# Performance work log

Measured on AMD Instinct MI355X. Metric: run time of the kernel, lower is better.

The kernel has to match this reference:

```python
import jax, jax.numpy as jnp
import numpy as np

B, D, H, W = 16, 512, 64, 64
K = 64  # clusters
EPS = 1e-12  # torch F.normalize eps


def _l2norm(v, axis):
    n = jnp.linalg.norm(v, axis=axis, keepdims=True)
    return v / jnp.maximum(n, EPS)


def setup_inputs() -> dict:
    key = jax.random.key(0)
    k1, k2, k3, k4 = jax.random.split(key, 4)
    x = jax.random.normal(k1, (B, D, H, W), dtype=jnp.float32)
    # conv weight/bias are independent trainable params after init; sample them
    centers = jax.random.uniform(k2, (K, D), dtype=jnp.float32)
    conv_w = 2.0 * 100.0 * centers + 0.01 * jax.random.normal(k3, (K, D), dtype=jnp.float32)
    conv_b = -100.0 * jnp.linalg.norm(centers, axis=1) + 0.01 * jax.random.normal(k4, (K,), dtype=jnp.float32)
    return {"x": x, "conv_w": conv_w, "conv_b": conv_b, "centers": centers}


def reference(x, conv_w, conv_b, centers):
    b = x.shape[0]
    x_flat = x.reshape(b, D, -1)                       # (B, D, N)
    # 1x1 conv == per-location linear over channels
    logits = jnp.einsum('bdn,kd->bkn', x_flat, conv_w) + conv_b[None, :, None]
    w = jax.nn.softmax(logits, axis=1)                 # softmax over clusters
    # vlad[b,k,d] = sum_n w[b,k,n]*(x[b,d,n] - c[k,d])
    #            = (w @ x^T)[b,k,d] - (sum_n w[b,k,n]) * c[k,d]
    wx = jnp.einsum('bkn,bdn->bkd', w, x_flat)         # (B, K, D)
    wsum = jnp.sum(w, axis=-1)                          # (B, K)
    vlad = wx - wsum[:, :, None] * centers[None]        # (B, K, D)
    vlad = _l2norm(vlad, axis=2)                        # intra-normalize
    vlad = vlad.reshape(b, -1)
    vlad = _l2norm(vlad, axis=1)                        # global L2
    return vlad
```

## Files before the change

### kernel.cpp

```cpp
#include <hip/hip_runtime.h>
#include <hip/hip_bf16.h>
#include <math.h>

#define B_ 16
#define D_ 512
#define N_ 4096
#define K_ 64

typedef __attribute__((ext_vector_type(8))) short bfrag;
typedef __attribute__((ext_vector_type(4))) float f32x4;

static __device__ __forceinline__ float bf2f(unsigned short u) {
    return __uint_as_float(((unsigned)u) << 16);
}
static __device__ __forceinline__ unsigned short f2bf(float v) {
    __hip_bfloat16 h = __float2bfloat16(v);
    union { __hip_bfloat16 h; unsigned short u; } cv; cv.h = h; return cv.u;
}
static __device__ __forceinline__ void split3(float v, unsigned short& h,
                                              unsigned short& m, unsigned short& l) {
    h = f2bf(v); float r1 = v - bf2f(h);
    m = f2bf(r1); float r2 = r1 - bf2f(m);
    l = f2bf(r2);
}
static __device__ __forceinline__ void split2(float v, unsigned short& h,
                                              unsigned short& l) {
    h = f2bf(v); l = f2bf(v - bf2f(h));
}
#define MFMA(a, b, c) __builtin_amdgcn_mfma_f32_16x16x32_bf16((a), (b), (c), 0, 0, 0)

__global__ __launch_bounds__(256) void k_prep(
    const float* __restrict__ conv_w, unsigned short* __restrict__ cwL)
{
    const int i = blockIdx.x * 256 + threadIdx.x;
    const float4 v = *(const float4*)&conv_w[i * 4];
    const float vv[4] = {v.x, v.y, v.z, v.w};
    unsigned short h[4], m[4], l[4];
    #pragma unroll
    for (int j = 0; j < 4; ++j) split3(vv[j], h[j], m[j], l[j]);
    *(ushort4*)&cwL[0 * (K_ * D_) + i * 4] = make_ushort4(h[0], h[1], h[2], h[3]);
    *(ushort4*)&cwL[1 * (K_ * D_) + i * 4] = make_ushort4(m[0], m[1], m[2], m[3]);
    *(ushort4*)&cwL[2 * (K_ * D_) + i * 4] = make_ushort4(l[0], l[1], l[2], l[3]);
}

__global__ __launch_bounds__(256) void k_logits_softmax(
    const float* __restrict__ x, const unsigned short* __restrict__ cwL,
    const float* __restrict__ conv_b,
    unsigned short* __restrict__ wh, unsigned short* __restrict__ wl,
    float* __restrict__ wsumbuf)
{
    const int b   = blockIdx.x >> 5;
    const int n0  = (blockIdx.x & 31) * 128;
    const int tid  = threadIdx.x;
    const int w    = tid >> 6;
    const int lane = tid & 63;
    const int q = lane >> 4;
    const int c = lane & 15;
    const int ktb = (w & 1) * 32;
    const int ntb = (w >> 1) * 64;

    __shared__ unsigned short cws[3][64][40];
    __shared__ unsigned short xs[3][128][40];
    __shared__ float redm[2][128];
    __shared__ float reds[2][128];

    f32x4 acc[2][4];
    #pragma unroll
    for (int kt = 0; kt < 2; ++kt)
        #pragma unroll
        for (int nt = 0; nt < 4; ++nt) acc[kt][nt] = (f32x4){0.f, 0.f, 0.f, 0.f};

    const float* xb = x + (size_t)b * D_ * N_ + n0;

    const int ks = tid >> 2;
    const int d8 = (tid & 3) * 8;
    const int xn = tid & 127;
    const int xd = (tid >> 7) * 4;

    float px[16];
    uint4 pcw[3];

    auto load_step = [&](int d0) {
        #pragma unroll
        for (int lv = 0; lv < 3; ++lv)
            pcw[lv] = *(const uint4*)&cwL[lv * (K_ * D_) + ks * D_ + d0 + d8];
        #pragma unroll
        for (int i = 0; i < 4; ++i)
            #pragma unroll
            for (int r = 0; r < 4; ++r)
                px[i * 4 + r] = xb[(size_t)(d0 + 8 * i + xd + r) * N_ + xn];
    };

    load_step(0);

    for (int s = 0; s < 16; ++s) {
        #pragma unroll
        for (int lv = 0; lv < 3; ++lv)
            *(uint4*)&cws[lv][ks][d8] = pcw[lv];
        #pragma unroll
        for (int i = 0; i < 4; ++i) {
            unsigned short h[4], m[4], l[4];
            #pragma unroll
            for (int r = 0; r < 4; ++r) split3(px[i * 4 + r], h[r], m[r], l[r]);
            const int dg = 8 * i + xd;
            *(ushort4*)&xs[0][xn][dg] = make_ushort4(h[0], h[1], h[2], h[3]);
            *(ushort4*)&xs[1][xn][dg] = make_ushort4(m[0], m[1], m[2], m[3]);
            *(ushort4*)&xs[2][xn][dg] = make_ushort4(l[0], l[1], l[2], l[3]);
        }
        __syncthreads();

        if (s < 15) load_step((s + 1) * 32);

        bfrag af[2][3];
        #pragma unroll
        for (int kt = 0; kt < 2; ++kt)
            #pragma unroll
            for (int lv = 0; lv < 3; ++lv)
                af[kt][lv] = *(const bfrag*)&cws[lv][ktb + kt * 16 + c][q * 8];
        #pragma unroll
        for (int nt = 0; nt < 4; ++nt) {
            bfrag bf[3];
            #pragma unroll
            for (int lv = 0; lv < 3; ++lv)
                bf[lv] = *(const bfrag*)&xs[lv][ntb + nt * 16 + c][q * 8];
            #pragma unroll
            for (int kt = 0; kt < 2; ++kt) {
                f32x4 a = acc[kt][nt];
                a = MFMA(af[kt][0], bf[0], a);
                a = MFMA(af[kt][0], bf[1], a);
                a = MFMA(af[kt][1], bf[0], a);
                a = MFMA(af[kt][1], bf[1], a);
                a = MFMA(af[kt][0], bf[2], a);
                a = MFMA(af[kt][2], bf[0], a);
                acc[kt][nt] = a;
            }
        }
        __syncthreads();
    }

    #pragma unroll
    for (int kt = 0; kt < 2; ++kt)
        #pragma unroll
        for (int r = 0; r < 4; ++r) {
            const float bias = conv_b[ktb + kt * 16 + q * 4 + r];
            #pragma unroll
            for (int nt = 0; nt < 4; ++nt) acc[kt][nt][r] += bias;
        }

    float mloc[4];
    #pragma unroll
    for (int nt = 0; nt < 4; ++nt) {
        float m = acc[0][nt][0];
        #pragma unroll
        for (int kt = 0; kt < 2; ++kt)
            #pragma unroll
            for (int r = 0; r < 4; ++r) m = fmaxf(m, acc[kt][nt][r]);
        m = fmaxf(m, __shfl_xor(m, 16));
        m = fmaxf(m, __shfl_xor(m, 32));
        mloc[nt] = m;
    }
    if (q == 0)
        #pragma unroll
        for (int nt = 0; nt < 4; ++nt) redm[w & 1][ntb + nt * 16 + c] = mloc[nt];
    __syncthreads();
    float mall[4];
    #pragma unroll
    for (int nt = 0; nt < 4; ++nt)
        mall[nt] = fmaxf(redm[0][ntb + nt * 16 + c], redm[1][ntb + nt * 16 + c]);

    float sloc[4] = {0.f, 0.f, 0.f, 0.f};
    #pragma unroll
    for (int nt = 0; nt < 4; ++nt) {
        #pragma unroll
        for (int kt = 0; kt < 2; ++kt)
            #pragma unroll
            for (int r = 0; r < 4; ++r) {
                const float e = __expf(acc[kt][nt][r] - mall[nt]);
                acc[kt][nt][r] = e;
                sloc[nt] += e;
            }
        sloc[nt] += __shfl_xor(sloc[nt], 16);
        sloc[nt] += __shfl_xor(sloc[nt], 32);
    }
    if (q == 0)
        #pragma unroll
        for (int nt = 0; nt < 4; ++nt) reds[w & 1][ntb + nt * 16 + c] = sloc[nt];
    __syncthreads();

    float wacc[2][4] = {{0.f, 0.f, 0.f, 0.f}, {0.f, 0.f, 0.f, 0.f}};
    #pragma unroll
    for (int nt = 0; nt < 4; ++nt) {
        const float inv = 1.0f / (reds[0][ntb + nt * 16 + c] + reds[1][ntb + nt * 16 + c]);
        #pragma unroll
        for (int kt = 0; kt < 2; ++kt)
            #pragma unroll
            for (int r = 0; r < 4; ++r) {
                const float v = acc[kt][nt][r] * inv;
                unsigned short hi, lo;
                split2(v, hi, lo);
                const size_t idx = ((size_t)b * K_ + ktb + kt * 16 + q * 4 + r) * N_
                                 + n0 + ntb + nt * 16 + c;
                wh[idx] = hi;
                wl[idx] = lo;
                wacc[kt][r] += v;
            }
    }
    #pragma unroll
    for (int msk = 1; msk < 16; msk <<= 1)
        #pragma unroll
        for (int kt = 0; kt < 2; ++kt)
            #pragma unroll
            for (int r = 0; r < 4; ++r)
                wacc[kt][r] += __shfl_xor(wacc[kt][r], msk);
    if (c == 0)
        #pragma unroll
        for (int kt = 0; kt < 2; ++kt)
            #pragma unroll
            for (int r = 0; r < 4; ++r)
                atomicAdd(&wsumbuf[b * K_ + ktb + kt * 16 + q * 4 + r], wacc[kt][r]);
}

__global__ __launch_bounds__(256) void k_wx(
    const float* __restrict__ x, const unsigned short* __restrict__ wh,
    const unsigned short* __restrict__ wl, float* __restrict__ vlad)
{
    const int nc = blockIdx.x & 7;
    const int dc = (blockIdx.x >> 3) & 3;
    const int b  = blockIdx.x >> 5;
    const int tid  = threadIdx.x;
    const int w    = tid >> 6;
    const int lane = tid & 63;
    const int q = lane >> 4;
    const int c = lane & 15;
    const int ktb = (w & 1) * 32;
    const int dtb = (w >> 1) * 64;

    __shared__ unsigned short ws2[2][64][40];
    __shared__ unsigned short xs2[2][128][40];

    f32x4 acc[2][4];
    #pragma unroll
    for (int kt = 0; kt < 2; ++kt)
        #pragma unroll
        for (int dt = 0; dt < 4; ++dt) acc[kt][dt] = (f32x4){0.f, 0.f, 0.f, 0.f};

    const float* xb = x + (size_t)b * D_ * N_ + (size_t)dc * 128 * N_;
    const unsigned short* whb = wh + (size_t)b * K_ * N_;
    const unsigned short* wlb = wl + (size_t)b * K_ * N_;

    const int wk = tid >> 2;
    const int wn = (tid & 3) * 8;
    const int xd = tid >> 3;
    const int xn = (tid & 7) * 4;

    uint4 pw[2];
    float px[16];

    auto load_step = [&](int n0) {
        pw[0] = *(const uint4*)&whb[(size_t)wk * N_ + n0 + wn];
        pw[1] = *(const uint4*)&wlb[(size_t)wk * N_ + n0 + wn];
        #pragma unroll
        for (int i = 0; i < 4; ++i) {
            const float4 v = *(const float4*)&xb[(size_t)(i * 32 + xd) * N_ + n0 + xn];
            px[i * 4 + 0] = v.x; px[i * 4 + 1] = v.y;
            px[i * 4 + 2] = v.z; px[i * 4 + 3] = v.w;
        }
    };

    const int nbase = nc * 512;
    load_step(nbase);

    for (int s = 0; s < 16; ++s) {
        *(uint4*)&ws2[0][wk][wn] = pw[0];
        *(uint4*)&ws2[1][wk][wn] = pw[1];
        #pragma unroll
        for (int i = 0; i < 4; ++i) {
            unsigned short h[4], l[4];
            #pragma unroll
            for (int j = 0; j < 4; ++j) split2(px[i * 4 + j], h[j], l[j]);
            *(ushort4*)&xs2[0][i * 32 + xd][xn] = make_ushort4(h[0], h[1], h[2], h[3]);
            *(ushort4*)&xs2[1][i * 32 + xd][xn] = make_ushort4(l[0], l[1], l[2], l[3]);
        }
        __syncthreads();

        if (s < 15) load_step(nbase + (s + 1) * 32);

        bfrag afh[2], afl[2];
        #pragma unroll
        for (int kt = 0; kt < 2; ++kt) {
            afh[kt] = *(const bfrag*)&ws2[0][ktb + kt * 16 + c][q * 8];
            afl[kt] = *(const bfrag*)&ws2[1][ktb + kt * 16 + c][q * 8];
        }
        #pragma unroll
        for (int dt = 0; dt < 4; ++dt) {
            const bfrag bh = *(const bfrag*)&xs2[0][dtb + dt * 16 + c][q * 8];
            const bfrag bl = *(const bfrag*)&xs2[1][dtb + dt * 16 + c][q * 8];
            #pragma unroll
            for (int kt = 0; kt < 2; ++kt) {
                f32x4 a = acc[kt][dt];
                a = MFMA(afh[kt], bh, a);
                a = MFMA(afh[kt], bl, a);
                a = MFMA(afl[kt], bh, a);
                acc[kt][dt] = a;
            }
        }
        __syncthreads();
    }

    #pragma unroll
    for (int kt = 0; kt < 2; ++kt)
        #pragma unroll
        for (int dt = 0; dt < 4; ++dt)
            #pragma unroll
            for (int r = 0; r < 4; ++r) {
                const int k = ktb + kt * 16 + q * 4 + r;
                const int d = dc * 128 + dtb + dt * 16 + c;
                atomicAdd(&vlad[((size_t)b * K_ + k) * D_ + d], acc[kt][dt][r]);
            }
}

__global__ __launch_bounds__(256) void k_norm(
    const float* __restrict__ wsumbuf, const float* __restrict__ vlad,
    const float* __restrict__ centers, float* __restrict__ out)
{
    const int b = blockIdx.x >> 6;
    const int k = blockIdx.x & 63;
    const int tid = threadIdx.x;

    const float wsum = wsumbuf[b * K_ + k];

    const float* vr = vlad + ((size_t)b * K_ + k) * D_;
    const float* cr = centers + k * D_;
    const float v0 = vr[tid]       - wsum * cr[tid];
    const float v1 = vr[tid + 256] - wsum * cr[tid + 256];

    float ss = v0 * v0 + v1 * v1;
    __shared__ float red2[4];
    #pragma unroll
    for (int off = 32; off > 0; off >>= 1) ss += __shfl_down(ss, off, 64);
    if ((tid & 63) == 0) red2[tid >> 6] = ss;
    __syncthreads();
    const float nrm = sqrtf(red2[0] + red2[1] + red2[2] + red2[3]);
    const float scale = 1.0f / (8.0f * fmaxf(nrm, 1e-12f));

    float* outr = out + ((size_t)b * K_ + k) * D_;
    outr[tid]       = v0 * scale;
    outr[tid + 256] = v1 * scale;
}

extern "C" void kernel_launch(void* const* d_in, const int* in_sizes, int n_in,
                              void* d_out, int out_size, void* d_ws, size_t ws_size,
                              hipStream_t stream) {
    const float* x       = (const float*)d_in[0];
    const float* conv_w  = (const float*)d_in[1];
    const float* conv_b  = (const float*)d_in[2];
    const float* centers = (const float*)d_in[3];
    float* out = (float*)d_out;

    char* wsb = (char*)d_ws;
    float* vlad            = (float*)wsb;
    float* wsumbuf         = (float*)(wsb + (2u << 20));
    unsigned short* wh     = (unsigned short*)(wsb + (3u << 20));
    unsigned short* wl     = (unsigned short*)(wsb + (11u << 20));
    unsigned short* cwL    = (unsigned short*)(wsb + (19u << 20));

    hipMemsetAsync(vlad, 0, (2u << 20) + 4096, stream);

    k_prep<<<32, 256, 0, stream>>>(conv_w, cwL);
    k_logits_softmax<<<B_ * 32, 256, 0, stream>>>(x, cwL, conv_b, wh, wl, wsumbuf);
    k_wx<<<B_ * 4 * 8, 256, 0, stream>>>(x, wh, wl, vlad);
    k_norm<<<B_ * K_, 256, 0, stream>>>(wsumbuf, vlad, centers, out);
}
```

Measured before the change: 261.2 us.

## Halve tile sizes to double grid and drop register prefetch pipelining

Both GEMM kernels now use smaller per-block tiles: the logits/softmax kernel covers 64 positions per block instead of 128, and the wx kernel covers 256 positions per block instead of 512. This doubles the number of blocks to 1024 in each kernel, to fill the MI355X's CUs better. The register-level software prefetch of the next step's global loads is also removed, which cuts register pressure and should raise occupancy. The trade-off is that global-load latency is no longer overlapped with MFMA work inside a block, and the wx kernel issues twice as many atomic accumulations into vlad.

```diff
diff --git a/kernel.cpp b/kernel.cpp
--- a/kernel.cpp
+++ b/kernel.cpp
@@ -49,67 +49,53 @@
     unsigned short* __restrict__ wh, unsigned short* __restrict__ wl,
     float* __restrict__ wsumbuf)
 {
-    const int b   = blockIdx.x >> 5;
-    const int n0  = (blockIdx.x & 31) * 128;
+    const int b   = blockIdx.x >> 6;
+    const int n0  = (blockIdx.x & 63) * 64;
     const int tid  = threadIdx.x;
     const int w    = tid >> 6;
     const int lane = tid & 63;
     const int q = lane >> 4;
     const int c = lane & 15;
     const int ktb = (w & 1) * 32;
-    const int ntb = (w >> 1) * 64;
+    const int ntb = (w >> 1) * 32;
 
     __shared__ unsigned short cws[3][64][40];
-    __shared__ unsigned short xs[3][128][40];
-    __shared__ float redm[2][128];
-    __shared__ float reds[2][128];
-
-    f32x4 acc[2][4];
+    __shared__ unsigned short xs[3][64][40];
+    __shared__ float redm[2][64];
+    __shared__ float reds[2][64];
+
+    f32x4 acc[2][2];
     #pragma unroll
     for (int kt = 0; kt < 2; ++kt)
         #pragma unroll
-        for (int nt = 0; nt < 4; ++nt) acc[kt][nt] = (f32x4){0.f, 0.f, 0.f, 0.f};
+        for (int nt = 0; nt < 2; ++nt) acc[kt][nt] = (f32x4){0.f, 0.f, 0.f, 0.f};
 
     const float* xb = x + (size_t)b * D_ * N_ + n0;
 
     const int ks = tid >> 2;
     const int d8 = (tid & 3) * 8;
-    const int xn = tid & 127;
-    const int xd = (tid >> 7) * 4;
-
-    float px[16];
-    uint4 pcw[3];
-
-    auto load_step = [&](int d0) {
+
+    for (int d0 = 0; d0 < D_; d0 += 32) {
         #pragma unroll
         for (int lv = 0; lv < 3; ++lv)
-            pcw[lv] = *(const uint4*)&cwL[lv * (K_ * D_) + ks * D_ + d0 + d8];
-        #pragma unroll
-        for (int i = 0; i < 4; ++i)
-            #pragma unroll
-            for (int r = 0; r < 4; ++r)
-                px[i * 4 + r] = xb[(size_t)(d0 + 8 * i + xd + r) * N_ + xn];
-    };
-
-    load_step(0);
-
-    for (int s = 0; s < 16; ++s) {
-        #pragma unroll
-        for (int lv = 0; lv < 3; ++lv)
-            *(uint4*)&cws[lv][ks][d8] = pcw[lv];
-        #pragma unroll
-        for (int i = 0; i < 4; ++i) {
+            *(uint4*)&cws[lv][ks][d8] =
+                *(const uint4*)&cwL[lv * (K_ * D_) + ks * D_ + d0 + d8];
+        #pragma unroll
+        for (int i = 0; i < 2; ++i) {
+            const int s   = i * 256 + tid;
+            const int xn  = s & 63;
+            const int dg4 = (s >> 6) * 4;
             unsigned short h[4], m[4], l[4];
             #pragma unroll
-            for (int r = 0; r < 4; ++r) split3(px[i * 4 + r], h[r], m[r], l[r]);
-            const int dg = 8 * i + xd;
-            *(ushort4*)&xs[0][xn][dg] = make_ushort4(h[0], h[1], h[2], h[3]);
-            *(ushort4*)&xs[1][xn][dg] = make_ushort4(m[0], m[1], m[2], m[3]);
-            *(ushort4*)&xs[2][xn][dg] = make_ushort4(l[0], l[1], l[2], l[3]);
+            for (int r = 0; r < 4; ++r) {
+                const float v = xb[(size_t)(d0 + dg4 + r) * N_ + xn];
+                split3(v, h[r], m[r], l[r]);
+            }
+            *(ushort4*)&xs[0][xn][dg4] = make_ushort4(h[0], h[1], h[2], h[3]);
+            *(ushort4*)&xs[1][xn][dg4] = make_ushort4(m[0], m[1], m[2], m[3]);
+            *(ushort4*)&xs[2][xn][dg4] = make_ushort4(l[0], l[1], l[2], l[3]);
         }
         __syncthreads();
-
-        if (s < 15) load_step((s + 1) * 32);
 
         bfrag af[2][3];
         #pragma unroll
@@ -118,7 +104,7 @@
             for (int lv = 0; lv < 3; ++lv)
                 af[kt][lv] = *(const bfrag*)&cws[lv][ktb + kt * 16 + c][q * 8];
         #pragma unroll
-        for (int nt = 0; nt < 4; ++nt) {
+        for (int nt = 0; nt < 2; ++nt) {
             bfrag bf[3];
             #pragma unroll
             for (int lv = 0; lv < 3; ++lv)
@@ -144,12 +130,12 @@
         for (int r = 0; r < 4; ++r) {
             const float bias = conv_b[ktb + kt * 16 + q * 4 + r];
             #pragma unroll
-            for (int nt = 0; nt < 4; ++nt) acc[kt][nt][r] += bias;
-        }
-
-    float mloc[4];
-    #pragma unroll
-    for (int nt = 0; nt < 4; ++nt) {
+            for (int nt = 0; nt < 2; ++nt) acc[kt][nt][r] += bias;
+        }
+
+    float mloc[2];
+    #pragma unroll
+    for (int nt = 0; nt < 2; ++nt) {
         float m = acc[0][nt][0];
         #pragma unroll
         for (int kt = 0; kt < 2; ++kt)
@@ -161,16 +147,16 @@
     }
     if (q == 0)
         #pragma unroll
-        for (int nt = 0; nt < 4; ++nt) redm[w & 1][ntb + nt * 16 + c] = mloc[nt];
+        for (int nt = 0; nt < 2; ++nt) redm[w & 1][ntb + nt * 16 + c] = mloc[nt];
     __syncthreads();
-    float mall[4];
-    #pragma unroll
-    for (int nt = 0; nt < 4; ++nt)
+    float mall[2];
+    #pragma unroll
+    for (int nt = 0; nt < 2; ++nt)
         mall[nt] = fmaxf(redm[0][ntb + nt * 16 + c], redm[1][ntb + nt * 16 + c]);
 
-    float sloc[4] = {0.f, 0.f, 0.f, 0.f};
-    #pragma unroll
-    for (int nt = 0; nt < 4; ++nt) {
+    float sloc[2] = {0.f, 0.f};
+    #pragma unroll
+    for (int nt = 0; nt < 2; ++nt) {
         #pragma unroll
         for (int kt = 0; kt < 2; ++kt)
             #pragma unroll
@@ -184,12 +170,12 @@
     }
     if (q == 0)
         #pragma unroll
-        for (int nt = 0; nt < 4; ++nt) reds[w & 1][ntb + nt * 16 + c] = sloc[nt];
+        for (int nt = 0; nt < 2; ++nt) reds[w & 1][ntb + nt * 16 + c] = sloc[nt];
     __syncthreads();
 
     float wacc[2][4] = {{0.f, 0.f, 0.f, 0.f}, {0.f, 0.f, 0.f, 0.f}};
     #pragma unroll
-    for (int nt = 0; nt < 4; ++nt) {
+    for (int nt = 0; nt < 2; ++nt) {
         const float inv = 1.0f / (reds[0][ntb + nt * 16 + c] + reds[1][ntb + nt * 16 + c]);
         #pragma unroll
         for (int kt = 0; kt < 2; ++kt)
@@ -224,9 +210,9 @@
     const float* __restrict__ x, const unsigned short* __restrict__ wh,
     const unsigned short* __restrict__ wl, float* __restrict__ vlad)
 {
-    const int nc = blockIdx.x & 7;
-    const int dc = (blockIdx.x >> 3) & 3;
-    const int b  = blockIdx.x >> 5;
+    const int nc = blockIdx.x & 15;
+    const int dc = (blockIdx.x >> 4) & 3;
+    const int b  = blockIdx.x >> 6;
     const int tid  = threadIdx.x;
     const int w    = tid >> 6;
     const int lane = tid & 63;
@@ -253,37 +239,21 @@
     const int xd = tid >> 3;
     const int xn = (tid & 7) * 4;
 
-    uint4 pw[2];
-    float px[16];
-
-    auto load_step = [&](int n0) {
-        pw[0] = *(const uint4*)&whb[(size_t)wk * N_ + n0 + wn];
-        pw[1] = *(const uint4*)&wlb[(size_t)wk * N_ + n0 + wn];
+    const int nbase = nc * 256;
+    for (int n0 = nbase; n0 < nbase + 256; n0 += 32) {
+        *(uint4*)&ws2[0][wk][wn] = *(const uint4*)&whb[(size_t)wk * N_ + n0 + wn];
+        *(uint4*)&ws2[1][wk][wn] = *(const uint4*)&wlb[(size_t)wk * N_ + n0 + wn];
         #pragma unroll
         for (int i = 0; i < 4; ++i) {
             const float4 v = *(const float4*)&xb[(size_t)(i * 32 + xd) * N_ + n0 + xn];
-            px[i * 4 + 0] = v.x; px[i * 4 + 1] = v.y;
-            px[i * 4 + 2] = v.z; px[i * 4 + 3] = v.w;
-        }
-    };
-
-    const int nbase = nc * 512;
-    load_step(nbase);
-
-    for (int s = 0; s < 16; ++s) {
-        *(uint4*)&ws2[0][wk][wn] = pw[0];
-        *(uint4*)&ws2[1][wk][wn] = pw[1];
-        #pragma unroll
-        for (int i = 0; i < 4; ++i) {
+            const float vv[4] = {v.x, v.y, v.z, v.w};
             unsigned short h[4], l[4];
             #pragma unroll
-            for (int j = 0; j < 4; ++j) split2(px[i * 4 + j], h[j], l[j]);
+            for (int j = 0; j < 4; ++j) split2(vv[j], h[j], l[j]);
             *(ushort4*)&xs2[0][i * 32 + xd][xn] = make_ushort4(h[0], h[1], h[2], h[3]);
             *(ushort4*)&xs2[1][i * 32 + xd][xn] = make_ushort4(l[0], l[1], l[2], l[3]);
         }
         __syncthreads();
-
-        if (s < 15) load_step(nbase + (s + 1) * 32);
 
         bfrag afh[2], afl[2];
         #pragma unroll
@@ -367,7 +337,7 @@
     hipMemsetAsync(vlad, 0, (2u << 20) + 4096, stream);
 
     k_prep<<<32, 256, 0, stream>>>(conv_w, cwL);
-    k_logits_softmax<<<B_ * 32, 256, 0, stream>>>(x, cwL, conv_b, wh, wl, wsumbuf);
-    k_wx<<<B_ * 4 * 8, 256, 0, stream>>>(x, wh, wl, vlad);
+    k_logits_softmax<<<B_ * 64, 256, 0, stream>>>(x, cwL, conv_b, wh, wl, wsumbuf);
+    k_wx<<<B_ * 4 * 16, 256, 0, stream>>>(x, wh, wl, vlad);
     k_norm<<<B_ * K_, 256, 0, stream>>>(wsumbuf, vlad, centers, out);
 }
```

Measured after the change: 265.6 us. No clear change (+1.7%).

## Swizzle x tile layout in LDS and drop register prefetch pipelining

Applied to the files above, without the earlier changes.

The logits kernel now stores the split x tile in shared memory with an XOR swizzle on the d-offset, keyed by row, to avoid bank conflicts on the transposed writes and the MFMA fragment reads. Both GEMM kernels drop their register-level software prefetch: loads now happen inside the loop right before the LDS store instead of overlapping with the previous step's MFMAs. This frees registers and may raise occupancy, but exposes global load latency within each step.

```diff
diff --git a/kernel.cpp b/kernel.cpp
--- a/kernel.cpp
+++ b/kernel.cpp
@@ -74,42 +74,31 @@
 
     const int ks = tid >> 2;
     const int d8 = (tid & 3) * 8;
-    const int xn = tid & 127;
-    const int xd = (tid >> 7) * 4;
-
-    float px[16];
-    uint4 pcw[3];
-
-    auto load_step = [&](int d0) {
+
+    for (int d0 = 0; d0 < D_; d0 += 32) {
         #pragma unroll
         for (int lv = 0; lv < 3; ++lv)
-            pcw[lv] = *(const uint4*)&cwL[lv * (K_ * D_) + ks * D_ + d0 + d8];
-        #pragma unroll
-        for (int i = 0; i < 4; ++i)
-            #pragma unroll
-            for (int r = 0; r < 4; ++r)
-                px[i * 4 + r] = xb[(size_t)(d0 + 8 * i + xd + r) * N_ + xn];
-    };
-
-    load_step(0);
-
-    for (int s = 0; s < 16; ++s) {
-        #pragma unroll
-        for (int lv = 0; lv < 3; ++lv)
-            *(uint4*)&cws[lv][ks][d8] = pcw[lv];
+            *(uint4*)&cws[lv][ks][d8] =
+                *(const uint4*)&cwL[lv * (K_ * D_) + ks * D_ + d0 + d8];
         #pragma unroll
         for (int i = 0; i < 4; ++i) {
+            const int s  = i * 256 + tid;
+            const int xn = s & 127;
+            const int j  = s >> 7;
+            const int Cs = ((j >> 1) ^ ((xn >> 3) & 3));
+            const int dsw = (Cs * 2 + (j & 1)) * 4;
+            const int dg4 = j * 4;
             unsigned short h[4], m[4], l[4];
             #pragma unroll
-            for (int r = 0; r < 4; ++r) split3(px[i * 4 + r], h[r], m[r], l[r]);
-            const int dg = 8 * i + xd;
-            *(ushort4*)&xs[0][xn][dg] = make_ushort4(h[0], h[1], h[2], h[3]);
-            *(ushort4*)&xs[1][xn][dg] = make_ushort4(m[0], m[1], m[2], m[3]);
-            *(ushort4*)&xs[2][xn][dg] = make_ushort4(l[0], l[1], l[2], l[3]);
+            for (int r = 0; r < 4; ++r) {
+                const float v = xb[(size_t)(d0 + dg4 + r) * N_ + xn];
+                split3(v, h[r], m[r], l[r]);
+            }
+            *(ushort4*)&xs[0][xn][dsw] = make_ushort4(h[0], h[1], h[2], h[3]);
+            *(ushort4*)&xs[1][xn][dsw] = make_ushort4(m[0], m[1], m[2], m[3]);
+            *(ushort4*)&xs[2][xn][dsw] = make_ushort4(l[0], l[1], l[2], l[3]);
         }
         __syncthreads();
-
-        if (s < 15) load_step((s + 1) * 32);
 
         bfrag af[2][3];
         #pragma unroll
@@ -119,10 +108,12 @@
                 af[kt][lv] = *(const bfrag*)&cws[lv][ktb + kt * 16 + c][q * 8];
         #pragma unroll
         for (int nt = 0; nt < 4; ++nt) {
+            const int row = ntb + nt * 16 + c;
+            const int qs  = (q ^ ((row >> 3) & 3)) * 8;
             bfrag bf[3];
             #pragma unroll
             for (int lv = 0; lv < 3; ++lv)
-                bf[lv] = *(const bfrag*)&xs[lv][ntb + nt * 16 + c][q * 8];
+                bf[lv] = *(const bfrag*)&xs[lv][row][qs];
             #pragma unroll
             for (int kt = 0; kt < 2; ++kt) {
                 f32x4 a = acc[kt][nt];
@@ -253,37 +244,21 @@
     const int xd = tid >> 3;
     const int xn = (tid & 7) * 4;
 
-    uint4 pw[2];
-    float px[16];
-
-    auto load_step = [&](int n0) {
-        pw[0] = *(const uint4*)&whb[(size_t)wk * N_ + n0 + wn];
-        pw[1] = *(const uint4*)&wlb[(size_t)wk * N_ + n0 + wn];
+    const int nbase = nc * 512;
+    for (int n0 = nbase; n0 < nbase + 512; n0 += 32) {
+        *(uint4*)&ws2[0][wk][wn] = *(const uint4*)&whb[(size_t)wk * N_ + n0 + wn];
+        *(uint4*)&ws2[1][wk][wn] = *(const uint4*)&wlb[(size_t)wk * N_ + n0 + wn];
         #pragma unroll
         for (int i = 0; i < 4; ++i) {
             const float4 v = *(const float4*)&xb[(size_t)(i * 32 + xd) * N_ + n0 + xn];
-            px[i * 4 + 0] = v.x; px[i * 4 + 1] = v.y;
-            px[i * 4 + 2] = v.z; px[i * 4 + 3] = v.w;
-        }
-    };
-
-    const int nbase = nc * 512;
-    load_step(nbase);
-
-    for (int s = 0; s < 16; ++s) {
-        *(uint4*)&ws2[0][wk][wn] = pw[0];
-        *(uint4*)&ws2[1][wk][wn] = pw[1];
-        #pragma unroll
-        for (int i = 0; i < 4; ++i) {
+            const float vv[4] = {v.x, v.y, v.z, v.w};
             unsigned short h[4], l[4];
             #pragma unroll
-            for (int j = 0; j < 4; ++j) split2(px[i * 4 + j], h[j], l[j]);
+            for (int j = 0; j < 4; ++j) split2(vv[j], h[j], l[j]);
             *(ushort4*)&xs2[0][i * 32 + xd][xn] = make_ushort4(h[0], h[1], h[2], h[3]);
             *(ushort4*)&xs2[1][i * 32 + xd][xn] = make_ushort4(l[0], l[1], l[2], l[3]);
         }
         __syncthreads();
-
-        if (s < 15) load_step(nbase + (s + 1) * 32);
 
         bfrag afh[2], afl[2];
         #pragma unroll
```

Result: faster. 237.4 us (-9.1%).
